# Kernel optimization log

Hardware: AMD Instinct MI355X
Metric: run time of the kernel (lower is better)

Reference implementation:

```python
import jax, jax.numpy as jnp
import numpy as np

ROI_SIZE = 14  # hard-coded in the torch module


def _bilinear(feature, x, y):
    """feature: [B,C,H,W]; x, y: arbitrary (matching) shape S of sample coords.
    Returns [B, C, *S]. Matches torch code: corner indices are clamped BEFORE
    the interpolation weights are computed from them."""
    H, W = feature.shape[-2:]
    y1 = jnp.clip(jnp.floor(y).astype(jnp.int32), 0, H - 1)
    y2 = jnp.clip(jnp.floor(y).astype(jnp.int32) + 1, 0, H - 1)
    x1 = jnp.clip(jnp.floor(x).astype(jnp.int32), 0, W - 1)
    x2 = jnp.clip(jnp.floor(x).astype(jnp.int32) + 1, 0, W - 1)
    wx_lo = x - x1  # weight toward x2 column
    wx_hi = x2 - x  # weight toward x1 column
    wy_lo = y - y1
    wy_hi = y2 - y
    p = feature[:, :, y1, x1] * wx_hi + feature[:, :, y1, x2] * wx_lo
    q = feature[:, :, y2, x1] * wx_hi + feature[:, :, y2, x2] * wx_lo
    return p * wy_hi + q * wy_lo


def setup_inputs() -> dict:
    key = jax.random.key(0)
    kf, k1, k2, k3, k4 = jax.random.split(key, 5)
    B, C, H, W, R = 1, 256, 200, 320, 128
    feature = jax.random.normal(kf, (B, C, H, W), dtype=jnp.float32)
    y1 = jax.random.uniform(k1, (R,), minval=0.0, maxval=H * 0.5)
    x1 = jax.random.uniform(k2, (R,), minval=0.0, maxval=W * 0.5)
    hh = jax.random.uniform(k3, (R,), minval=8.0, maxval=H * 0.45)
    ww = jax.random.uniform(k4, (R,), minval=8.0, maxval=W * 0.45)
    rois = jnp.stack([y1, x1, y1 + hh, x1 + ww], axis=-1).astype(jnp.float32)
    return {"feature": feature, "rois": rois}


def reference(feature, rois):
    R = rois.shape[0]
    B, C, H, W = feature.shape
    sh = (rois[:, 2] - rois[:, 0]) / ROI_SIZE  # [R] bin height stride
    sw = (rois[:, 3] - rois[:, 1]) / ROI_SIZE  # [R] bin width stride
    m = jnp.arange(ROI_SIZE, dtype=rois.dtype)
    y_base = rois[:, 0:1] + sh[:, None] * m  # [R, M]
    x_base = rois[:, 1:2] + sw[:, None] * m  # [R, N]
    frac = jnp.array([1.0 / 3.0, 2.0 / 3.0], dtype=rois.dtype)
    ys = y_base[:, :, None] + sh[:, None, None] * frac  # [R, M, 2]
    xs = x_base[:, :, None] + sw[:, None, None] * frac  # [R, N, 2]
    # all 4 (y, x) sample-point combos per bin -> [R, M, N, 2, 2]
    yy = jnp.broadcast_to(ys[:, :, None, :, None], (R, ROI_SIZE, ROI_SIZE, 2, 2))
    xx = jnp.broadcast_to(xs[:, None, :, None, :], (R, ROI_SIZE, ROI_SIZE, 2, 2))
    samples = _bilinear(feature, xx, yy)  # [B, C, R, M, N, 2, 2]
    # Faithful to torch.max(tensor) with NO dim: global max over B, C, R and
    # the 4 sample points, giving one scalar per bin (m, n).
    bin_max = jnp.max(samples, axis=(0, 1, 2, 5, 6))  # [M, N]
    return jnp.broadcast_to(bin_max, (R, C, ROI_SIZE, ROI_SIZE))
```

## Files before the change

### kernel.cpp

```cpp
#include <hip/hip_runtime.h>
#include <float.h>

#define CC 256
#define HH 200
#define WW 320
#define HW (HH * WW)
#define MM 14
#define SPAN_MAX 144
#define SPAN_PAD 145
#define NCH 8
#define CG 4
#define CPB (CC / CG)

__global__ void roi_init(float* __restrict__ binmax) {
    int t = blockIdx.x * blockDim.x + threadIdx.x;
    if (t < MM * MM) binmax[t] = -FLT_MAX;
}

__device__ inline void atomicMaxF(float* addr, float val) {
    if (val >= 0.0f) {
        atomicMax((int*)addr, __float_as_int(val));
    } else {
        atomicMin((unsigned int*)addr, __float_as_uint(val));
    }
}

__global__ __launch_bounds__(256, 8) void roi_reduce(
    const float* __restrict__ feature,
    const float* __restrict__ rois,
    float* __restrict__ binmax)
{
    const int bid = blockIdx.x;
    const int cg  = bid & (CG - 1);
    const int rm  = bid >> 2;
    const int m   = rm % MM;
    const int r   = rm / MM;
    const int tid = threadIdx.x;
    const int cbase = cg * CPB;

    const float ry1 = rois[r * 4 + 0];
    const float rx1 = rois[r * 4 + 1];
    const float ry2 = rois[r * 4 + 2];
    const float rx2 = rois[r * 4 + 3];
    const float sh = (ry2 - ry1) * (1.0f / 14.0f);
    const float sw = (rx2 - rx1) * (1.0f / 14.0f);
    const float f13 = 1.0f / 3.0f, f23 = 2.0f / 3.0f;

    const float yA = ry1 + sh * (float)m + sh * f13;
    const float yB = ry1 + sh * (float)m + sh * f23;
    const int y1A = min(max((int)floorf(yA), 0), HH - 1);
    const int y2A = min(max((int)floorf(yA) + 1, 0), HH - 1);
    const int y1B = min(max((int)floorf(yB), 0), HH - 1);
    const int y2B = min(max((int)floorf(yB) + 1, 0), HH - 1);
    const float wyloA = yA - (float)y1A, wyhiA = (float)y2A - yA;
    const float wyloB = yB - (float)y1B, wyhiB = (float)y2B - yB;

    const float xmin = rx1 + sw * f13;
    const float xmax = rx1 + sw * 13.0f + sw * f23;
    int xlo = min(max((int)floorf(xmin), 0), WW - 1);
    int xhi = min(max((int)floorf(xmax) + 1, 0), WW - 1);
    int span = xhi - xlo + 1;
    if (span > SPAN_MAX) span = SPAN_MAX;

    const int s  = tid % 56;
    const int cs = tid / 56;
    const int n  = s >> 2;
    const int j  = (s >> 1) & 1;
    const int i  = s & 1;
    const bool active = (tid < 224);

    float wxlo = 0.f, wxhi = 0.f, wylo = 0.f, wyhi = 0.f;
    int c0 = 0, c1 = 0, ra = 0, rb = 1;
    if (active) {
        float x = rx1 + sw * (float)n + sw * (j ? f23 : f13);
        int x1c = min(max((int)floorf(x), 0), WW - 1);
        int x2c = min(max((int)floorf(x) + 1, 0), WW - 1);
        wxlo = x - (float)x1c;
        wxhi = (float)x2c - x;
        c0 = min(max(x1c - xlo, 0), span - 1);
        c1 = min(max(x2c - xlo, 0), span - 1);
        if (i == 0) { ra = 0; rb = 1; wylo = wyloA; wyhi = wyhiA; }
        else        { ra = 2; rb = 3; wylo = wyloB; wyhi = wyhiB; }
    }

    __shared__ float tile[NCH][4][SPAN_PAD];
    __shared__ float pmax[224];

    const int rg   = tid >> 6;
    const int lane = tid & 63;
    const int myrow = (rg == 0) ? y1A : (rg == 1) ? y2A : (rg == 2) ? y1B : y2B;
    const int rowoff = myrow * WW + xlo;

    float lmax = -FLT_MAX;

    for (int cc = 0; cc < CPB; cc += NCH) {
        const float* src = feature + (cbase + cc) * HW + rowoff;
        __syncthreads();
        for (int col = lane; col < span; col += 64) {
            float tmp[NCH];
            #pragma unroll
            for (int ch = 0; ch < NCH; ++ch) tmp[ch] = src[ch * HW + col];
            #pragma unroll
            for (int ch = 0; ch < NCH; ++ch) tile[ch][rg][col] = tmp[ch];
        }
        __syncthreads();
        if (active) {
            #pragma unroll
            for (int q = 0; q < 2; ++q) {
                const int ch = cs * 2 + q;
                float v11 = tile[ch][ra][c0];
                float v12 = tile[ch][ra][c1];
                float v21 = tile[ch][rb][c0];
                float v22 = tile[ch][rb][c1];
                float p = v11 * wxhi + v12 * wxlo;
                float q2 = v21 * wxhi + v22 * wxlo;
                lmax = fmaxf(lmax, p * wyhi + q2 * wylo);
            }
        }
    }

    if (active) pmax[tid] = lmax;
    __syncthreads();
    if (tid < MM) {
        float v = -FLT_MAX;
        #pragma unroll
        for (int c4 = 0; c4 < 4; ++c4)
            #pragma unroll
            for (int q4 = 0; q4 < 4; ++q4)
                v = fmaxf(v, pmax[c4 * 56 + tid * 4 + q4]);
        atomicMaxF(&binmax[m * MM + tid], v);
    }
}

__global__ __launch_bounds__(256) void roi_bcast(
    const float* __restrict__ binmax, float4* __restrict__ out, int total4)
{
    __shared__ float4 b4[49];
    int t = threadIdx.x;
    if (t < 49) b4[t] = ((const float4*)binmax)[t];
    __syncthreads();
    int idx = blockIdx.x * 256 + t;
    if (idx < total4) out[idx] = b4[idx % 49];
}

extern "C" void kernel_launch(void* const* d_in, const int* in_sizes, int n_in,
                              void* d_out, int out_size, void* d_ws, size_t ws_size,
                              hipStream_t stream) {
    const float* feature = (const float*)d_in[0];
    const float* rois    = (const float*)d_in[1];
    float* binmax = (float*)d_ws;
    float* out    = (float*)d_out;

    const int R = in_sizes[1] / 4;

    roi_init<<<1, 256, 0, stream>>>(binmax);
    roi_reduce<<<R * MM * CG, 256, 0, stream>>>(feature, rois, binmax);

    const int total4 = out_size / 4;
    roi_bcast<<<(total4 + 255) / 256, 256, 0, stream>>>(binmax, (float4*)out, total4);
}
```

Baseline: 145.1 us.

## Double-buffer ROI row tiles with async global-to-LDS loads and halve channel groups

Replaces the register-staged row copies with `__builtin_amdgcn_global_load_lds` 16-byte direct-to-LDS loads. The row start is aligned down to 4 floats, and the loads go into a double-buffered tile so the next channel chunk is fetched while the current one is interpolated. Channel groups per ROI row drop from 4 to 2, which halves the block count, lowers the occupancy hint and gives each block more rounds to pipeline. The partial max reduction now uses wave shuffles. The kernel also assumes the second bilinear column is always `c0+1`, which holds only while sample x-coordinates stay away from the right edge.

```diff
diff --git a/kernel.cpp b/kernel.cpp
--- a/kernel.cpp
+++ b/kernel.cpp
@@ -6,11 +6,14 @@
 #define WW 320
 #define HW (HH * WW)
 #define MM 14
-#define SPAN_MAX 144
-#define SPAN_PAD 145
+#define SPAN 148
 #define NCH 8
-#define CG 4
+#define CG 2
 #define CPB (CC / CG)
+#define ROUNDS (CPB / NCH)
+
+typedef __attribute__((address_space(1))) const float GF;
+typedef __attribute__((address_space(3))) float LF;
 
 __global__ void roi_init(float* __restrict__ binmax) {
     int t = blockIdx.x * blockDim.x + threadIdx.x;
@@ -25,17 +28,22 @@
     }
 }
 
-__global__ __launch_bounds__(256, 8) void roi_reduce(
+__global__ __launch_bounds__(256, 4) void roi_reduce(
     const float* __restrict__ feature,
     const float* __restrict__ rois,
     float* __restrict__ binmax)
 {
+    __shared__ float tile[2][NCH][4][SPAN];
+    __shared__ float pmax[4][MM];
+
     const int bid = blockIdx.x;
     const int cg  = bid & (CG - 1);
-    const int rm  = bid >> 2;
+    const int rm  = bid >> 1;
     const int m   = rm % MM;
     const int r   = rm / MM;
-    const int tid = threadIdx.x;
+    const int tid  = threadIdx.x;
+    const int w    = tid >> 6;
+    const int lane = tid & 63;
     const int cbase = cg * CPB;
 
     const float ry1 = rois[r * 4 + 0];
@@ -57,78 +65,76 @@
 
     const float xmin = rx1 + sw * f13;
     const float xmax = rx1 + sw * 13.0f + sw * f23;
-    int xlo = min(max((int)floorf(xmin), 0), WW - 1);
-    int xhi = min(max((int)floorf(xmax) + 1, 0), WW - 1);
+    const int xlo = (min(max((int)floorf(xmin), 0), WW - 1)) & ~3;
+    const int xhi = min(max((int)floorf(xmax) + 1, 0), WW - 1);
     int span = xhi - xlo + 1;
-    if (span > SPAN_MAX) span = SPAN_MAX;
+    if (span > SPAN) span = SPAN;
+    const int nlanes = (span + 3) >> 2;
 
-    const int s  = tid % 56;
-    const int cs = tid / 56;
-    const int n  = s >> 2;
-    const int j  = (s >> 1) & 1;
-    const int i  = s & 1;
-    const bool active = (tid < 224);
+    const int myrow = (w == 0) ? y1A : (w == 1) ? y2A : (w == 2) ? y1B : y2B;
+    const float* gbase = feature + (cbase * HW + myrow * WW + xlo) + lane * 4;
+
+    const bool active = lane < 56;
+    const int n = lane >> 2;
+    const int j = (lane >> 1) & 1;
+    const int i = lane & 1;
 
     float wxlo = 0.f, wxhi = 0.f, wylo = 0.f, wyhi = 0.f;
-    int c0 = 0, c1 = 0, ra = 0, rb = 1;
+    int c0 = 0, ra = 0;
     if (active) {
         float x = rx1 + sw * (float)n + sw * (j ? f23 : f13);
         int x1c = min(max((int)floorf(x), 0), WW - 1);
         int x2c = min(max((int)floorf(x) + 1, 0), WW - 1);
         wxlo = x - (float)x1c;
         wxhi = (float)x2c - x;
-        c0 = min(max(x1c - xlo, 0), span - 1);
-        c1 = min(max(x2c - xlo, 0), span - 1);
-        if (i == 0) { ra = 0; rb = 1; wylo = wyloA; wyhi = wyhiA; }
-        else        { ra = 2; rb = 3; wylo = wyloB; wyhi = wyhiB; }
+        c0 = min(max(x1c - xlo, 0), SPAN - 2);
+        if (i == 0) { ra = 0; wylo = wyloA; wyhi = wyhiA; }
+        else        { ra = 2; wylo = wyloB; wyhi = wyhiB; }
     }
 
-    __shared__ float tile[NCH][4][SPAN_PAD];
-    __shared__ float pmax[224];
+    auto stage = [&](int rd, int b) {
+        const float* g = gbase + rd * (NCH * HW);
+        if (lane < nlanes) {
+            #pragma unroll
+            for (int ch = 0; ch < NCH; ++ch) {
+                __builtin_amdgcn_global_load_lds(
+                    (GF*)(g + ch * HW), (LF*)&tile[b][ch][w][0], 16, 0, 0);
+            }
+        }
+    };
 
-    const int rg   = tid >> 6;
-    const int lane = tid & 63;
-    const int myrow = (rg == 0) ? y1A : (rg == 1) ? y2A : (rg == 2) ? y1B : y2B;
-    const int rowoff = myrow * WW + xlo;
+    stage(0, 0);
+    float lmax = -FLT_MAX;
+    int buf = 0;
 
-    float lmax = -FLT_MAX;
-
-    for (int cc = 0; cc < CPB; cc += NCH) {
-        const float* src = feature + (cbase + cc) * HW + rowoff;
+    for (int rd = 0; rd < ROUNDS; ++rd) {
         __syncthreads();
-        for (int col = lane; col < span; col += 64) {
-            float tmp[NCH];
-            #pragma unroll
-            for (int ch = 0; ch < NCH; ++ch) tmp[ch] = src[ch * HW + col];
-            #pragma unroll
-            for (int ch = 0; ch < NCH; ++ch) tile[ch][rg][col] = tmp[ch];
-        }
-        __syncthreads();
+        if (rd + 1 < ROUNDS) stage(rd + 1, buf ^ 1);
         if (active) {
             #pragma unroll
             for (int q = 0; q < 2; ++q) {
-                const int ch = cs * 2 + q;
-                float v11 = tile[ch][ra][c0];
-                float v12 = tile[ch][ra][c1];
-                float v21 = tile[ch][rb][c0];
-                float v22 = tile[ch][rb][c1];
-                float p = v11 * wxhi + v12 * wxlo;
-                float q2 = v21 * wxhi + v22 * wxlo;
-                lmax = fmaxf(lmax, p * wyhi + q2 * wylo);
+                const float* rp = &tile[buf][w * 2 + q][ra][0];
+                float v11 = rp[c0];
+                float v12 = rp[c0 + 1];
+                float v21 = rp[SPAN + c0];
+                float v22 = rp[SPAN + c0 + 1];
+                float p  = v11 * wxhi + v12 * wxlo;
+                float qq = v21 * wxhi + v22 * wxlo;
+                lmax = fmaxf(lmax, p * wyhi + qq * wylo);
             }
         }
+        buf ^= 1;
     }
 
-    if (active) pmax[tid] = lmax;
+    float v = lmax;
+    v = fmaxf(v, __shfl_xor(v, 1));
+    v = fmaxf(v, __shfl_xor(v, 2));
+    if (active && (lane & 3) == 0) pmax[w][n] = v;
     __syncthreads();
     if (tid < MM) {
-        float v = -FLT_MAX;
-        #pragma unroll
-        for (int c4 = 0; c4 < 4; ++c4)
-            #pragma unroll
-            for (int q4 = 0; q4 < 4; ++q4)
-                v = fmaxf(v, pmax[c4 * 56 + tid * 4 + q4]);
-        atomicMaxF(&binmax[m * MM + tid], v);
+        float vv = fmaxf(fmaxf(pmax[0][tid], pmax[1][tid]),
+                         fmaxf(pmax[2][tid], pmax[3][tid]));
+        atomicMaxF(&binmax[m * MM + tid], vv);
     }
 }
 
```

Result: slower. 165.4 us (+14.0%).
